# Kernel optimization log

Measured on AMD Instinct MI355X. Metric: run time of the kernel, lower is better.

The kernel has to match this reference:

```python
import jax, jax.numpy as jnp
import numpy as np

L = 2        # n_layer
D = 1024     # hidden_size
H = 8        # n_head
DK = D // H  # head_dim = 128
DV = D // H
T = 2048     # max_seq_length
B = 4
INTER = 2816 # fla GatedMLP: int(1024*4*2/3)=2730 rounded up to multiple of 256
EPS = 1e-6


def rmsnorm(x, w):
    return x * jax.lax.rsqrt(jnp.mean(x * x, axis=-1, keepdims=True) + EPS) * w


def l2norm(x):
    return x * jax.lax.rsqrt(jnp.sum(x * x, axis=-1, keepdims=True) + EPS)


def delta_attn(x, Wq, Wk, Wv, Wb, Wo, onorm_w):
    # x: [B, T, D]
    b, t, _ = x.shape
    q = jax.nn.silu((x @ Wq).reshape(b, t, H, DK))
    k = jax.nn.silu((x @ Wk).reshape(b, t, H, DK))
    q = l2norm(q)
    k = l2norm(k)
    v = jax.nn.silu((x @ Wv).reshape(b, t, H, DV))
    beta = jax.nn.sigmoid(x @ Wb) * 2.0  # [B,T,H], allow_neg_eigval=True
    # time-major for scan
    qt = q.transpose(1, 0, 2, 3)  # [T,B,H,DK]
    kt = k.transpose(1, 0, 2, 3)
    vt = v.transpose(1, 0, 2, 3)
    bt = beta.transpose(1, 0, 2)  # [T,B,H]

    def step(S, inps):
        qi, ki, vi, bi = inps
        # delta rule: S_t = S_{t-1} + beta_t * k_t (v_t - S_{t-1}^T k_t)^T
        pred = jnp.einsum('bhkv,bhk->bhv', S, ki)
        S = S + bi[..., None, None] * ki[..., :, None] * (vi - pred)[..., None, :]
        o = jnp.einsum('bhkv,bhk->bhv', S, qi)
        return S, o

    S0 = jnp.zeros((b, H, DK, DV), x.dtype)
    _, o = jax.lax.scan(step, S0, (qt, kt, vt, bt))  # o: [T,B,H,DV]
    o = rmsnorm(o, onorm_w)  # per-head RMSNorm (use_gate=False)
    o = o.transpose(1, 0, 2, 3).reshape(b, t, H * DV)
    return o @ Wo


def setup_inputs() -> dict:
    key = jax.random.key(0)
    ks = jax.random.split(key, 13)
    s = 0.02
    f32 = jnp.float32
    return {
        'input_embeds': jax.random.normal(ks[0], (T, B, D), f32),
        'Wq': jax.random.normal(ks[1], (L, D, D), f32) * s,
        'Wk': jax.random.normal(ks[2], (L, D, D), f32) * s,
        'Wv': jax.random.normal(ks[3], (L, D, D), f32) * s,
        'Wb': jax.random.normal(ks[4], (L, D, H), f32) * s,
        'Wo': jax.random.normal(ks[5], (L, D, D), f32) * s,
        'onorm_w': jnp.ones((L, DV), f32) + jax.random.normal(ks[6], (L, DV), f32) * 0.02,
        'norm1_w': jnp.ones((L, D), f32) + jax.random.normal(ks[7], (L, D), f32) * 0.02,
        'norm2_w': jnp.ones((L, D), f32) + jax.random.normal(ks[8], (L, D), f32) * 0.02,
        'Wg': jax.random.normal(ks[9], (L, D, 2 * INTER), f32) * s,
        'Wd': jax.random.normal(ks[10], (L, INTER, D), f32) * s,
        'final_norm_w': jnp.ones((D,), f32) + jax.random.normal(ks[11], (D,), f32) * 0.02,
    }


def reference(input_embeds, Wq, Wk, Wv, Wb, Wo, onorm_w, norm1_w, norm2_w, Wg, Wd, final_norm_w):
    # wrapper transposes (T,B,D) -> (B,T,D)
    x = input_embeds.transpose(1, 0, 2)
    for l in range(L):
        h = rmsnorm(x, norm1_w[l])
        x = x + delta_attn(h, Wq[l], Wk[l], Wv[l], Wb[l], Wo[l], onorm_w[l])
        h = rmsnorm(x, norm2_w[l])
        gy = h @ Wg[l]
        g, y = jnp.split(gy, 2, axis=-1)
        x = x + (jax.nn.silu(g) * y) @ Wd[l]
    x = rmsnorm(x, final_norm_w)
    return x.transpose(1, 0, 2)  # back to (T,B,D)
```

## Files before the change

kernel.cpp:

```cpp
#include <hip/hip_runtime.h>
#include <hip/hip_bf16.h>
#include <cstdint>


typedef _Float16 f16;
typedef __attribute__((ext_vector_type(8))) _Float16 h8;
typedef __attribute__((ext_vector_type(4))) _Float16 h4;
typedef __attribute__((ext_vector_type(4))) float f4;

#define DEV __device__ __forceinline__

static constexpr int Bb_ = 4;
static constexpr int Hh  = 8;
static constexpr int Dd  = 1024;
static constexpr int Tt  = 2048;
static constexpr int NC  = 32;

DEV float siluf(float x) { return x / (1.f + expf(-x)); }
DEV int swz16(int row, int c) { return (c & 8) | ((c & 7) ^ (row & 7)); }

#define AS1(p) ((const __attribute__((address_space(1))) void*)(uintptr_t)(p))
#define AS3(p) ((__attribute__((address_space(3))) void*)(uint32_t)(uintptr_t)(p))

DEV h8 rd_sw(const f16* T, int row, int chunk) {
  return *(const h8*)(T + (((row << 3) | (chunk ^ (row & 7))) * 8));
}

template<int EPI, int BN>
__global__ __launch_bounds__(512, 2) void gemm2(const f16* __restrict__ A, const f16* __restrict__ Bt,
                                                void* __restrict__ C, int M, int N, int K, int gx) {
  __shared__ __align__(16) f16 ldsA[2][16384];
  __shared__ __align__(16) f16 ldsB[2][BN * 64];
  const int tid = threadIdx.x, lane = tid & 63, w = tid >> 6;
  const int l15 = lane & 15, l4 = lane >> 4;
  const int wr = w >> 2, wc = w & 3;
  const int nwg = gridDim.x;
  int flat = blockIdx.x;
  if ((nwg & 7) == 0) flat = (flat & 7) * (nwg >> 3) + (flat >> 3);
  const int bx = flat % gx, by = flat / gx;

  const f16* Ab = A + (size_t)by * 256 * K;
  const f16* Bb = Bt + (size_t)bx * BN * K;
  const int NT = K >> 6;
  constexpr int NCF = BN / 64;
  f4 acc[8][NCF] = {};

  const int r0 = tid >> 3;
  const size_t soff0 = (size_t)r0 * K + (size_t)(((tid & 7) ^ (r0 & 7)) * 8);
  const size_t soff1 = soff0 + (size_t)64 * K;
  const int dof = tid * 8;
  auto STG = [&](const f16* base, f16* dst) {
    __builtin_amdgcn_global_load_lds(AS1(base + soff0), AS3(dst + dof), 16, 0, 0);
    __builtin_amdgcn_global_load_lds(AS1(base + soff1), AS3(dst + 4096 + dof), 16, 0, 0);
  };

  STG(Bb, ldsB[0]);
  if (BN == 256) STG(Bb + (size_t)128 * K, ldsB[0] + 8192);
  STG(Ab, ldsA[0]);
  STG(Ab + (size_t)128 * K, ldsA[0] + 8192);
  if (NT > 1) {
    STG(Bb + 64, ldsB[1]);
    if (BN == 256) STG(Bb + (size_t)128 * K + 64, ldsB[1] + 8192);
    if (BN == 256) asm volatile("s_waitcnt vmcnt(4)");
    else           asm volatile("s_waitcnt vmcnt(2)");
  } else {
    asm volatile("s_waitcnt vmcnt(0)");
  }
  __builtin_amdgcn_s_barrier();

  for (int t = 0; t < NT; ++t) {
    const int cur = t & 1, nxt = cur ^ 1;
    const f16* cA = ldsA[cur];
    const f16* cB = ldsB[cur];
    h8 b[NCF][2];
    h8 a[2][2];
#pragma unroll
    for (int cf = 0; cf < NCF; ++cf)
#pragma unroll
      for (int ks = 0; ks < 2; ++ks)
        b[cf][ks] = rd_sw(cB, wc * (BN / 4) + cf * 16 + l15, ks * 4 + l4);
#pragma unroll
    for (int fr = 0; fr < 2; ++fr)
#pragma unroll
      for (int ks = 0; ks < 2; ++ks)
        a[fr][ks] = rd_sw(cA, wr * 128 + fr * 16 + l15, ks * 4 + l4);
    if (t + 1 < NT) STG(Ab + (t + 1) * 64, ldsA[nxt]);
    asm volatile("s_waitcnt lgkmcnt(0)");
    __builtin_amdgcn_s_setprio(1);
#pragma unroll
    for (int fr = 0; fr < 2; ++fr)
#pragma unroll
      for (int cf = 0; cf < NCF; ++cf)
#pragma unroll
        for (int ks = 0; ks < 2; ++ks)
          acc[fr][cf] = __builtin_amdgcn_mfma_f32_16x16x32_f16(a[fr][ks], b[cf][ks], acc[fr][cf], 0, 0, 0);
    __builtin_amdgcn_s_setprio(0);
    __builtin_amdgcn_s_barrier();
#pragma unroll
    for (int p = 1; p < 4; ++p) {
#pragma unroll
      for (int fr = 0; fr < 2; ++fr)
#pragma unroll
        for (int ks = 0; ks < 2; ++ks)
          a[fr][ks] = rd_sw(cA, wr * 128 + p * 32 + fr * 16 + l15, ks * 4 + l4);
      if (p == 1 && t + 1 < NT) STG(Ab + (size_t)128 * K + (t + 1) * 64, ldsA[nxt] + 8192);
      if (p == 2 && t + 2 < NT) STG(Bb + (t + 2) * 64, ldsB[cur]);
      if (BN == 256 && p == 3 && t + 2 < NT) STG(Bb + (size_t)128 * K + (t + 2) * 64, ldsB[cur] + 8192);
      asm volatile("s_waitcnt lgkmcnt(0)");
      __builtin_amdgcn_s_setprio(1);
#pragma unroll
      for (int fr = 0; fr < 2; ++fr)
#pragma unroll
        for (int cf = 0; cf < NCF; ++cf)
#pragma unroll
          for (int ks = 0; ks < 2; ++ks)
            acc[p * 2 + fr][cf] = __builtin_amdgcn_mfma_f32_16x16x32_f16(a[fr][ks], b[cf][ks], acc[p * 2 + fr][cf], 0, 0, 0);
      __builtin_amdgcn_s_setprio(0);
      if (p == 3) {
        if (t + 2 < NT) {
          if (BN == 256) asm volatile("s_waitcnt vmcnt(4)");
          else           asm volatile("s_waitcnt vmcnt(2)");
        } else if (t + 1 < NT) {
          asm volatile("s_waitcnt vmcnt(0)");
        }
      }
      __builtin_amdgcn_s_barrier();
    }
  }

#pragma unroll
  for (int fr = 0; fr < 8; ++fr) {
#pragma unroll
    for (int cf = 0; cf < NCF; ++cf) {
      const int row0 = by * 256 + wr * 128 + fr * 16 + l4 * 4;
      const int col = bx * BN + wc * (BN / 4) + cf * 16 + l15;
#pragma unroll
      for (int q = 0; q < 4; ++q) {
        const size_t idx = (size_t)(row0 + q) * N + col;
        const float v = acc[fr][cf][q];
        if (EPI == 0) ((float*)C)[idx] = v;
        if (EPI == 1) ((f16*)C)[idx] = (f16)((float)((f16*)C)[idx] + v);
        if (EPI == 2) ((f16*)C)[idx] = (f16)v;
      }
    }
  }
}

__global__ __launch_bounds__(512, 2) void gemmGLU(const f16* __restrict__ A, const f16* __restrict__ WgT,
                                                  f16* __restrict__ my, int K, int gx) {
  __shared__ __align__(16) f16 ldsA[2][16384];
  __shared__ __align__(16) f16 ldsG[2][8192];
  __shared__ __align__(16) f16 ldsY[2][8192];
  const int tid = threadIdx.x, lane = tid & 63, w = tid >> 6;
  const int l15 = lane & 15, l4 = lane >> 4;
  const int wr = w >> 2, wc = w & 3;
  const int nwg = gridDim.x;
  int flat = blockIdx.x;
  if ((nwg & 7) == 0) flat = (flat & 7) * (nwg >> 3) + (flat >> 3);
  const int bx = flat % gx, by = flat / gx;

  const f16* Ab = A + (size_t)by * 256 * K;
  const f16* Gb = WgT + (size_t)bx * 128 * K;
  const f16* Yb = WgT + (size_t)(2816 + bx * 128) * K;
  const int NT = K >> 6;
  f4 accG[8][2] = {}, accY[8][2] = {};

  const int r0 = tid >> 3;
  const size_t soff0 = (size_t)r0 * K + (size_t)(((tid & 7) ^ (r0 & 7)) * 8);
  const size_t soff1 = soff0 + (size_t)64 * K;
  const int dof = tid * 8;
  auto STG = [&](const f16* base, f16* dst) {
    __builtin_amdgcn_global_load_lds(AS1(base + soff0), AS3(dst + dof), 16, 0, 0);
    __builtin_amdgcn_global_load_lds(AS1(base + soff1), AS3(dst + 4096 + dof), 16, 0, 0);
  };

  STG(Gb, ldsG[0]);
  STG(Yb, ldsY[0]);
  STG(Ab, ldsA[0]);
  STG(Ab + (size_t)128 * K, ldsA[0] + 8192);
  if (NT > 1) {
    STG(Gb + 64, ldsG[1]);
    STG(Yb + 64, ldsY[1]);
    asm volatile("s_waitcnt vmcnt(4)");
  } else {
    asm volatile("s_waitcnt vmcnt(0)");
  }
  __builtin_amdgcn_s_barrier();

  for (int t = 0; t < NT; ++t) {
    const int cur = t & 1, nxt = cur ^ 1;
    const f16* cA = ldsA[cur];
    h8 bg[2][2], byv[2][2];
    h8 a[2][2];
#pragma unroll
    for (int cf = 0; cf < 2; ++cf)
#pragma unroll
      for (int ks = 0; ks < 2; ++ks) {
        bg[cf][ks] = rd_sw(ldsG[cur], wc * 32 + cf * 16 + l15, ks * 4 + l4);
        byv[cf][ks] = rd_sw(ldsY[cur], wc * 32 + cf * 16 + l15, ks * 4 + l4);
      }
#pragma unroll
    for (int fr = 0; fr < 2; ++fr)
#pragma unroll
      for (int ks = 0; ks < 2; ++ks)
        a[fr][ks] = rd_sw(cA, wr * 128 + fr * 16 + l15, ks * 4 + l4);
    if (t + 1 < NT) STG(Ab + (t + 1) * 64, ldsA[nxt]);
    asm volatile("s_waitcnt lgkmcnt(0)");
    __builtin_amdgcn_s_setprio(1);
#pragma unroll
    for (int fr = 0; fr < 2; ++fr)
#pragma unroll
      for (int cf = 0; cf < 2; ++cf)
#pragma unroll
        for (int ks = 0; ks < 2; ++ks) {
          accG[fr][cf] = __builtin_amdgcn_mfma_f32_16x16x32_f16(a[fr][ks], bg[cf][ks], accG[fr][cf], 0, 0, 0);
          accY[fr][cf] = __builtin_amdgcn_mfma_f32_16x16x32_f16(a[fr][ks], byv[cf][ks], accY[fr][cf], 0, 0, 0);
        }
    __builtin_amdgcn_s_setprio(0);
    __builtin_amdgcn_s_barrier();
#pragma unroll
    for (int p = 1; p < 4; ++p) {
#pragma unroll
      for (int fr = 0; fr < 2; ++fr)
#pragma unroll
        for (int ks = 0; ks < 2; ++ks)
          a[fr][ks] = rd_sw(cA, wr * 128 + p * 32 + fr * 16 + l15, ks * 4 + l4);
      if (p == 1 && t + 1 < NT) STG(Ab + (size_t)128 * K + (t + 1) * 64, ldsA[nxt] + 8192);
      if (p == 2 && t + 2 < NT) STG(Gb + (t + 2) * 64, ldsG[cur]);
      if (p == 3 && t + 2 < NT) STG(Yb + (t + 2) * 64, ldsY[cur]);
      asm volatile("s_waitcnt lgkmcnt(0)");
      __builtin_amdgcn_s_setprio(1);
#pragma unroll
      for (int fr = 0; fr < 2; ++fr)
#pragma unroll
        for (int cf = 0; cf < 2; ++cf)
#pragma unroll
          for (int ks = 0; ks < 2; ++ks) {
            accG[p * 2 + fr][cf] = __builtin_amdgcn_mfma_f32_16x16x32_f16(a[fr][ks], bg[cf][ks], accG[p * 2 + fr][cf], 0, 0, 0);
            accY[p * 2 + fr][cf] = __builtin_amdgcn_mfma_f32_16x16x32_f16(a[fr][ks], byv[cf][ks], accY[p * 2 + fr][cf], 0, 0, 0);
          }
      __builtin_amdgcn_s_setprio(0);
      if (p == 3) {
        if (t + 2 < NT) asm volatile("s_waitcnt vmcnt(4)");
        else if (t + 1 < NT) asm volatile("s_waitcnt vmcnt(0)");
      }
      __builtin_amdgcn_s_barrier();
    }
  }

#pragma unroll
  for (int fr = 0; fr < 8; ++fr) {
#pragma unroll
    for (int cf = 0; cf < 2; ++cf) {
      const int row0 = by * 256 + wr * 128 + fr * 16 + l4 * 4;
      const int col = bx * 128 + wc * 32 + cf * 16 + l15;
#pragma unroll
      for (int q = 0; q < 4; ++q)
        my[(size_t)(row0 + q) * 2816 + col] = (f16)(siluf(accG[fr][cf][q]) * accY[fr][cf][q]);
    }
  }
}

__global__ __launch_bounds__(256) void cvt_k(const float* __restrict__ in, f16* __restrict__ out) {
  const size_t i = ((size_t)blockIdx.x * 256 + threadIdx.x) * 8;
  const float4 a = *(const float4*)(in + i);
  const float4 b = *(const float4*)(in + i + 4);
  h8 o = {(f16)a.x, (f16)a.y, (f16)a.z, (f16)a.w, (f16)b.x, (f16)b.y, (f16)b.z, (f16)b.w};
  *(h8*)(out + i) = o;
}

template<int OUT_F16>
__global__ __launch_bounds__(256) void rmsnorm_k(const f16* __restrict__ x, const float* __restrict__ w,
                                                 void* __restrict__ out) {
  const int r = blockIdx.x, tid = threadIdx.x;
  const h4 xv = *(const h4*)(x + (size_t)r * 1024 + tid * 4);
  const float v0 = (float)xv[0], v1 = (float)xv[1], v2 = (float)xv[2], v3 = (float)xv[3];
  float ss = v0 * v0 + v1 * v1 + v2 * v2 + v3 * v3;
#pragma unroll
  for (int m = 1; m < 64; m <<= 1) ss += __shfl_xor(ss, m);
  __shared__ float red[4];
  if ((tid & 63) == 0) red[tid >> 6] = ss;
  __syncthreads();
  const float scale = rsqrtf((red[0] + red[1] + red[2] + red[3]) * (1.f / 1024.f) + 1e-6f);
  const float4 w4 = *(const float4*)(w + tid * 4);
  float o0 = v0 * scale * w4.x, o1 = v1 * scale * w4.y, o2 = v2 * scale * w4.z, o3 = v3 * scale * w4.w;
  if (OUT_F16) {
    h4 o = {(f16)o0, (f16)o1, (f16)o2, (f16)o3};
    *(h4*)((f16*)out + (size_t)r * 1024 + tid * 4) = o;
  } else {
    *(float4*)((float*)out + (size_t)r * 1024 + tid * 4) = make_float4(o0, o1, o2, o3);
  }
}

__global__ __launch_bounds__(256) void qkv_epi(const f16* __restrict__ qkv, f16* __restrict__ qb,
                                               f16* __restrict__ kb, f16* __restrict__ vb) {
  const int r = blockIdx.x, tid = threadIdx.x;
  const int head = tid >> 5, l32 = tid & 31;
  const int i = (r >> 2) & 63;
  const size_t src = (size_t)r * 3072 + head * 128 + l32 * 4;
  {
    const h4 v = *(const h4*)(qkv + src);
    float s0 = siluf((float)v[0]), s1 = siluf((float)v[1]), s2 = siluf((float)v[2]), s3 = siluf((float)v[3]);
    float ss = s0 * s0 + s1 * s1 + s2 * s2 + s3 * s3;
#pragma unroll
    for (int m = 1; m <= 16; m <<= 1) ss += __shfl_xor(ss, m);
    const float sc = rsqrtf(ss + 1e-6f);
    h4 o = {(f16)(s0 * sc), (f16)(s1 * sc), (f16)(s2 * sc), (f16)(s3 * sc)};
    const int c = l32 >> 1, off = (l32 & 1) * 4;
    *(h4*)(qb + (size_t)r * 1024 + head * 128 + swz16(i, c) * 8 + off) = o;
  }
  {
    const h4 v = *(const h4*)(qkv + src + 1024);
    float s0 = siluf((float)v[0]), s1 = siluf((float)v[1]), s2 = siluf((float)v[2]), s3 = siluf((float)v[3]);
    float ss = s0 * s0 + s1 * s1 + s2 * s2 + s3 * s3;
#pragma unroll
    for (int m = 1; m <= 16; m <<= 1) ss += __shfl_xor(ss, m);
    const float sc = rsqrtf(ss + 1e-6f);
    h4 o = {(f16)(s0 * sc), (f16)(s1 * sc), (f16)(s2 * sc), (f16)(s3 * sc)};
    const int c = l32 >> 1, off = (l32 & 1) * 4;
    *(h4*)(kb + (size_t)r * 1024 + head * 128 + swz16(i, c) * 8 + off) = o;
  }
  {
    const h4 v = *(const h4*)(qkv + (size_t)r * 3072 + 2048 + tid * 4);
    h4 o = {(f16)siluf((float)v[0]), (f16)siluf((float)v[1]), (f16)siluf((float)v[2]), (f16)siluf((float)v[3])};
    const int hd = tid >> 5, dh = (tid & 31) * 4;
    const int c = dh >> 3, off = dh & 7;
    *(h4*)(vb + (size_t)r * 1024 + hd * 128 + swz16(i, c) * 8 + off) = o;
  }
}

__global__ __launch_bounds__(256) void onorm_k(const f16* __restrict__ o, const float* __restrict__ w,
                                               f16* __restrict__ ob) {
  const int r = blockIdx.x, tid = threadIdx.x;
  const int head = tid >> 5, l32 = tid & 31;
  const size_t base = (size_t)r * 1024 + head * 128 + l32 * 4;
  const h4 xv = *(const h4*)(o + base);
  const float v0 = (float)xv[0], v1 = (float)xv[1], v2 = (float)xv[2], v3 = (float)xv[3];
  float ss = v0 * v0 + v1 * v1 + v2 * v2 + v3 * v3;
#pragma unroll
  for (int m = 1; m <= 16; m <<= 1) ss += __shfl_xor(ss, m);
  const float sc = rsqrtf(ss * (1.f / 128.f) + 1e-6f);
  const float4 w4 = *(const float4*)(w + l32 * 4);
  h4 out = {(f16)(v0 * sc * w4.x), (f16)(v1 * sc * w4.y), (f16)(v2 * sc * w4.z), (f16)(v3 * sc * w4.w)};
  *(h4*)(ob + base) = out;
}

__global__ __launch_bounds__(256) void beta_k(const f16* __restrict__ hb, const float* __restrict__ Wb,
                                              float* __restrict__ beta) {
  const int tid = threadIdx.x, lane = tid & 63, wv = tid >> 6;
  const int r = blockIdx.x * 4 + wv;
  const f16* row = hb + (size_t)r * 1024 + lane * 16;
  const h8 v0 = *(const h8*)(row);
  const h8 v1 = *(const h8*)(row + 8);
  const float* wb = Wb + (size_t)(lane * 16) * 8;
  float acc[8] = {};
#pragma unroll
  for (int e = 0; e < 8; ++e) {
    const float x0 = (float)v0[e], x1 = (float)v1[e];
    const float4 w0a = *(const float4*)(wb + e * 8);
    const float4 w0b = *(const float4*)(wb + e * 8 + 4);
    const float4 w1a = *(const float4*)(wb + (e + 8) * 8);
    const float4 w1b = *(const float4*)(wb + (e + 8) * 8 + 4);
    acc[0] += x0 * w0a.x + x1 * w1a.x;  acc[1] += x0 * w0a.y + x1 * w1a.y;
    acc[2] += x0 * w0a.z + x1 * w1a.z;  acc[3] += x0 * w0a.w + x1 * w1a.w;
    acc[4] += x0 * w0b.x + x1 * w1b.x;  acc[5] += x0 * w0b.y + x1 * w1b.y;
    acc[6] += x0 * w0b.z + x1 * w1b.z;  acc[7] += x0 * w0b.w + x1 * w1b.w;
  }
#pragma unroll
  for (int j = 0; j < 8; ++j)
#pragma unroll
    for (int m = 1; m < 64; m <<= 1) acc[j] += __shfl_xor(acc[j], m);
  if (lane == 0) {
#pragma unroll
    for (int j = 0; j < 8; ++j) beta[(size_t)r * 8 + j] = 2.f / (1.f + expf(-acc[j]));
  }
}

__global__ __launch_bounds__(256) void transpose_k(const float* __restrict__ W, f16* __restrict__ Wt,
                                                   int K, int N) {
  __shared__ float tile[32][33];
  const int n0 = blockIdx.x * 32, k0 = blockIdx.y * 32;
  const int tx = threadIdx.x & 31, ty = threadIdx.x >> 5;
#pragma unroll
  for (int i = 0; i < 32; i += 8) tile[ty + i][tx] = W[(size_t)(k0 + ty + i) * N + n0 + tx];
  __syncthreads();
#pragma unroll
  for (int i = 0; i < 32; i += 8) Wt[(size_t)(n0 + ty + i) * K + k0 + tx] = (f16)tile[tx][ty + i];
}

__global__ void fill_k(float* p, int n, float v) {
  const int i = blockIdx.x * 256 + threadIdx.x;
  if (i < n) p[i] = v;
}

DEV f4 mm16(const f16* A, int as, const f16* B, f4 c, int l15, int l4) {
  h4 a = *(const h4*)(A + l15 * as + l4 * 4);
  h4 b = *(const h4*)(B + l15 * 20 + l4 * 4);
  return __builtin_amdgcn_mfma_f32_16x16x16f16(a, b, c, 0, 0, 0);
}
DEV void wr_T(f16* slot, f4 acc, int l15, int l4, float sgn) {
  h4 v = {(f16)(sgn * acc[0]), (f16)(sgn * acc[1]), (f16)(sgn * acc[2]), (f16)(sgn * acc[3])};
  *(h4*)(slot + l15 * 20 + l4 * 4) = v;
}
DEV void wr_Tb(f16* Tb, int bi, int bj, f4 acc, const float* betas, int l15, int l4, float sgn) {
  const float bc = betas[bj * 16 + l15];
#pragma unroll
  for (int q = 0; q < 4; ++q)
    Tb[(bi * 16 + l4 * 4 + q) * 72 + bj * 16 + l15] = (f16)(sgn * acc[q] * bc);
}

__global__ __launch_bounds__(256) void phaseA(const f16* __restrict__ kb, const f16* __restrict__ qb,
                                              const f16* __restrict__ vb, const float* __restrict__ beta,
                                              f16* __restrict__ wbuf, f16* __restrict__ utbuf,
                                              f16* __restrict__ pbuf, f16* __restrict__ ktbuf) {
  const int blk = blockIdx.x;
  const int c = blk >> 5, bh = blk & 31;
  const int b = bh >> 3, h = bh & 7;
  const int tid = threadIdx.x, lane = tid & 63, wv = tid >> 6;
  const int l15 = lane & 15, l4 = lane >> 4;

  __shared__ __align__(16) f16 Ks[64 * 128];
  __shared__ __align__(16) f16 QVs[64 * 128];
  __shared__ __align__(16) f16 Abuf[64 * 68];
  __shared__ __align__(16) f16 Dr[4][16 * 20];
  __shared__ __align__(16) f16 Dt[4][16 * 20];
  __shared__ __align__(16) f16 Tp[3][16 * 20];
  __shared__ __align__(16) f16 Xp[3][16 * 20];
  __shared__ __align__(16) f16 Tb[64 * 72];
  __shared__ float betas[64];

  const size_t rowstr = (size_t)Bb_ * Dd;
  const size_t gbase = ((size_t)(c * 64) * Bb_ + b) * Dd + h * 128;

#pragma unroll
  for (int i = 0; i < 4; ++i) {
    const int ch = tid + i * 256;
    const int rr = ch >> 4, kc = ch & 15;
    *(h8*)(Ks + ch * 8) = *(const h8*)(kb + gbase + (size_t)rr * rowstr + kc * 8);
    *(h8*)(QVs + ch * 8) = *(const h8*)(qb + gbase + (size_t)rr * rowstr + kc * 8);
  }
  for (int i = tid; i < 64 * 72; i += 256) Tb[i] = (f16)0.f;
  if (tid < 64) betas[tid] = beta[((size_t)(c * 64 + tid) * Bb_ + b) * Hh + h];
  __syncthreads();

  f4 accS[4] = {}, accP[4] = {};
  const int arow = wv * 16 + l15;
#pragma unroll
  for (int kc = 0; kc < 4; ++kc) {
    const int c4 = kc * 4 + l4;
    const h8 aK = *(const h8*)(Ks + arow * 128 + swz16(arow, c4) * 8);
    const h8 aQ = *(const h8*)(QVs + arow * 128 + swz16(arow, c4) * 8);
#pragma unroll
    for (int f = 0; f < 4; ++f) {
      const int brow = f * 16 + l15;
      const h8 bK = *(const h8*)(Ks + brow * 128 + swz16(brow, c4) * 8);
      accS[f] = __builtin_amdgcn_mfma_f32_16x16x32_f16(aK, bK, accS[f], 0, 0, 0);
      accP[f] = __builtin_amdgcn_mfma_f32_16x16x32_f16(aQ, bK, accP[f], 0, 0, 0);
    }
  }
  const size_t pbase = (((size_t)bh * NC + c) * 64) * 64;
#pragma unroll
  for (int f = 0; f < 4; ++f) {
#pragma unroll
    for (int q = 0; q < 4; ++q) {
      const int i = wv * 16 + l4 * 4 + q;
      const int j = f * 16 + l15;
      Abuf[i * 68 + j] = (f16)((j < i) ? betas[i] * accS[f][q] : 0.f);
      pbuf[pbase + (size_t)i * 64 + j] = (f16)((j <= i) ? accP[f][q] : 0.f);
    }
  }
// ... 181 lines not shown
    if (c + 1 < NC) asm volatile("s_waitcnt vmcnt(12)" ::: "memory");
    else            asm volatile("s_waitcnt vmcnt(0)" ::: "memory");
#pragma unroll
    for (int f = 0; f < 2; ++f) {
      const h4 uu = f ? u1 : u0;
      h4 rw;
#pragma unroll
      for (int q = 0; q < 4; ++q) {
        const float rv = (float)uu[q] - accR[f][q];
        accR[f][q] = rv;
        rw[q] = (f16)rv;
      }
      *(h4*)(Rt + (f * 16 + l15) * 72 + wv * 16 + l4 * 4) = rw;
    }
    asm volatile("s_waitcnt lgkmcnt(0)" ::: "memory");
    __builtin_amdgcn_s_barrier();

#pragma unroll
    for (int kc = 0; kc < 2; ++kc) {
      const h8 aP = kc ? aP1 : aP0;
#pragma unroll
      for (int f = 0; f < 2; ++f) {
        const h8 bR = *(const h8*)(Rt + (f * 16 + l15) * 72 + kc * 32 + koff);
        accO[f] = __builtin_amdgcn_mfma_f32_16x16x32_f16(aP, bR, accO[f], 0, 0, 0);
      }
    }
#pragma unroll
    for (int f = 0; f < 2; ++f)
#pragma unroll
      for (int q = 0; q < 4; ++q) {
        const int i = wv * 16 + l4 * 4 + q;
        const int cc = f * 16 + l15;
        obuf[((size_t)(c * 64 + i) * Bb_ + b) * Dd + h * 128 + g * 32 + cc] = (f16)accO[f][q];
      }

#pragma unroll
    for (int kc = 0; kc < 2; ++kc) {
      const h8 aR0 = *(const h8*)(Rt + l15 * 72 + kc * 32 + koff);
      const h8 aR1 = *(const h8*)(Rt + (16 + l15) * 72 + kc * 32 + koff);
#pragma unroll
      for (int cf = 0; cf < 2; ++cf) {
        const int kcol = wv * 32 + cf * 16 + l15;
        const int c2 = kc * 4 + l4;
        const h8 bKv = *(const h8*)(Kts[cur] + kcol * 64 + (c2 ^ (kcol & 7)) * 8);
        macc[0][cf] = __builtin_amdgcn_mfma_f32_16x16x32_f16(aR0, bKv, macc[0][cf], 0, 0, 0);
        macc[1][cf] = __builtin_amdgcn_mfma_f32_16x16x32_f16(aR1, bKv, macc[1][cf], 0, 0, 0);
      }
    }
#pragma unroll
    for (int rf = 0; rf < 2; ++rf)
#pragma unroll
      for (int cf = 0; cf < 2; ++cf)
#pragma unroll
        for (int q = 0; q < 4; ++q) {
          const int cr = rf * 16 + l4 * 4 + q;
          const int kcol = wv * 32 + cf * 16 + l15;
          Ms[cr * 136 + kcol] = (f16)macc[rf][cf][q];
        }
  }
}

extern "C" void kernel_launch(void* const* d_in, const int* in_sizes, int n_in,
                              void* d_out, int out_size, void* d_ws, size_t ws_size,
                              hipStream_t stream) {
  (void)in_sizes; (void)n_in;
  const float* input = (const float*)d_in[0];
  const float* Wq = (const float*)d_in[1];
  const float* Wk = (const float*)d_in[2];
  const float* Wv = (const float*)d_in[3];
  const float* Wb = (const float*)d_in[4];
  const float* Wo = (const float*)d_in[5];
  const float* onw = (const float*)d_in[6];
  const float* n1w = (const float*)d_in[7];
  const float* n2w = (const float*)d_in[8];
  const float* Wg = (const float*)d_in[9];
  const float* Wd = (const float*)d_in[10];
  const float* fnw = (const float*)d_in[11];

  char* ws = (char*)d_ws;
  size_t off = 0;
  auto alloc = [&](size_t bytes) { void* p = ws + off; off += (bytes + 255) & ~(size_t)255; return p; };
  const size_t RD = 8192ull * 1024ull;
  f16*  x     = (f16*)alloc(RD * 2);
  f16*  hb    = (f16*)alloc(RD * 2);
  f16*  qb    = (f16*)alloc(RD * 2);
  f16*  kbuf  = (f16*)alloc(RD * 2);
  f16*  vbuf  = (f16*)alloc(RD * 2);
  float* beta = (float*)alloc(8192ull * 8 * 4);
  f16*  wbuf  = (f16*)alloc(RD * 2);
  f16*  utbuf = (f16*)alloc(RD * 2);
  f16*  ktbuf = (f16*)alloc(RD * 2);
  f16*  pbuf  = (f16*)alloc(32ull * 32 * 64 * 64 * 2);
  char* arena = (char*)alloc(3 * RD * 2);
  f16*  WqkvT = (f16*)alloc(3072ull * 1024 * 2);
  f16*  WoT   = (f16*)alloc(1024ull * 1024 * 2);
  f16*  WgT   = (f16*)alloc(5632ull * 1024 * 2);
  f16*  WdT   = (f16*)alloc(1024ull * 2816 * 2);
  if (off > ws_size) {
    fill_k<<<(out_size + 255) / 256, 256, 0, stream>>>((float*)d_out, out_size, 1.0e6f);
    return;
  }
  f16* qkvraw = (f16*)arena;
  f16* obuf = (f16*)arena;
  f16* my = qb;
  f16* ob = wbuf;

  cvt_k<<<4096, 256, 0, stream>>>(input, x);

  for (int l = 0; l < 2; ++l) {
    const size_t o2 = (size_t)l * 1024 * 1024;
    transpose_k<<<dim3(32, 32), 256, 0, stream>>>(Wq + o2, WqkvT, 1024, 1024);
    transpose_k<<<dim3(32, 32), 256, 0, stream>>>(Wk + o2, WqkvT + 1024ull * 1024, 1024, 1024);
    transpose_k<<<dim3(32, 32), 256, 0, stream>>>(Wv + o2, WqkvT + 2048ull * 1024, 1024, 1024);
    transpose_k<<<dim3(32, 32), 256, 0, stream>>>(Wo + o2, WoT, 1024, 1024);
    transpose_k<<<dim3(176, 32), 256, 0, stream>>>(Wg + (size_t)l * 1024 * 5632, WgT, 1024, 5632);
    transpose_k<<<dim3(32, 88), 256, 0, stream>>>(Wd + (size_t)l * 2816 * 1024, WdT, 2816, 1024);

    rmsnorm_k<1><<<8192, 256, 0, stream>>>(x, n1w + l * 1024, hb);
    gemm2<2, 128><<<32 * 24, 512, 0, stream>>>(hb, WqkvT, qkvraw, 8192, 3072, 1024, 24);
    beta_k<<<2048, 256, 0, stream>>>(hb, Wb + (size_t)l * 1024 * 8, beta);
    qkv_epi<<<8192, 256, 0, stream>>>(qkvraw, qb, kbuf, vbuf);
    phaseA<<<1024, 256, 0, stream>>>(kbuf, qb, vbuf, beta, wbuf, utbuf, pbuf, ktbuf);
    phaseB<<<128, 256, 0, stream>>>(qb, ktbuf, wbuf, utbuf, pbuf, obuf);
    onorm_k<<<8192, 256, 0, stream>>>(obuf, onw + l * 128, ob);
    gemm2<1, 128><<<32 * 8, 512, 0, stream>>>(ob, WoT, x, 8192, 1024, 1024, 8);

    rmsnorm_k<1><<<8192, 256, 0, stream>>>(x, n2w + l * 1024, hb);
    gemmGLU<<<32 * 22, 512, 0, stream>>>(hb, WgT, my, 1024, 22);
    gemm2<1, 128><<<32 * 8, 512, 0, stream>>>(my, WdT, x, 8192, 1024, 2816, 8);
  }
  rmsnorm_k<0><<<8192, 256, 0, stream>>>(x, fnw, d_out);
}
```

Baseline: 993.7 us.

## Fold RMSNorm into GEMM weights and row-scale epilogue; restructure GEMM K-loop

Removes the materialized normalized activation buffer. The norm weights are folded into the transposed projection weights, and a small kernel computes per-row inverse RMS scales. The QKV, GLU and beta GEMMs then apply that scale in their epilogue. The GEMM main loops are also restructured from four barrier-separated phases into two halves, with double register buffers and fewer lgkmcnt waits and barriers. This saves a full read/write pass over the activations but relies on the compiler to order LDS reads, since the explicit lgkmcnt waits are gone.

```diff
diff --git a/kernel.cpp b/kernel.cpp
--- a/kernel.cpp
+++ b/kernel.cpp
@@ -26,11 +26,12 @@
   return *(const h8*)(T + (((row << 3) | (chunk ^ (row & 7))) * 8));
 }
 
-template<int EPI, int BN>
+template<int EPI, int SC>
 __global__ __launch_bounds__(512, 2) void gemm2(const f16* __restrict__ A, const f16* __restrict__ Bt,
-                                                void* __restrict__ C, int M, int N, int K, int gx) {
+                                                void* __restrict__ C, const float* __restrict__ rs,
+                                                int M, int N, int K, int gx) {
   __shared__ __align__(16) f16 ldsA[2][16384];
-  __shared__ __align__(16) f16 ldsB[2][BN * 64];
+  __shared__ __align__(16) f16 ldsB[2][8192];
   const int tid = threadIdx.x, lane = tid & 63, w = tid >> 6;
   const int l15 = lane & 15, l4 = lane >> 4;
   const int wr = w >> 2, wc = w & 3;
@@ -40,10 +41,9 @@
   const int bx = flat % gx, by = flat / gx;
 
   const f16* Ab = A + (size_t)by * 256 * K;
-  const f16* Bb = Bt + (size_t)bx * BN * K;
+  const f16* Bb = Bt + (size_t)bx * 128 * K;
   const int NT = K >> 6;
-  constexpr int NCF = BN / 64;
-  f4 acc[8][NCF] = {};
+  f4 acc[8][2] = {};
 
   const int r0 = tid >> 3;
   const size_t soff0 = (size_t)r0 * K + (size_t)(((tid & 7) ^ (r0 & 7)) * 8);
@@ -55,14 +55,11 @@
   };
 
   STG(Bb, ldsB[0]);
-  if (BN == 256) STG(Bb + (size_t)128 * K, ldsB[0] + 8192);
   STG(Ab, ldsA[0]);
   STG(Ab + (size_t)128 * K, ldsA[0] + 8192);
   if (NT > 1) {
     STG(Bb + 64, ldsB[1]);
-    if (BN == 256) STG(Bb + (size_t)128 * K + 64, ldsB[1] + 8192);
-    if (BN == 256) asm volatile("s_waitcnt vmcnt(4)");
-    else           asm volatile("s_waitcnt vmcnt(2)");
+    asm volatile("s_waitcnt vmcnt(2)");
   } else {
     asm volatile("s_waitcnt vmcnt(0)");
   }
@@ -72,73 +69,83 @@
     const int cur = t & 1, nxt = cur ^ 1;
     const f16* cA = ldsA[cur];
     const f16* cB = ldsB[cur];
-    h8 b[NCF][2];
-    h8 a[2][2];
-#pragma unroll
-    for (int cf = 0; cf < NCF; ++cf)
+    h8 b[2][2], aX[2][2], aY[2][2];
+#pragma unroll
+    for (int cf = 0; cf < 2; ++cf)
 #pragma unroll
       for (int ks = 0; ks < 2; ++ks)
-        b[cf][ks] = rd_sw(cB, wc * (BN / 4) + cf * 16 + l15, ks * 4 + l4);
+        b[cf][ks] = rd_sw(cB, wc * 32 + cf * 16 + l15, ks * 4 + l4);
 #pragma unroll
     for (int fr = 0; fr < 2; ++fr)
 #pragma unroll
       for (int ks = 0; ks < 2; ++ks)
-        a[fr][ks] = rd_sw(cA, wr * 128 + fr * 16 + l15, ks * 4 + l4);
-    if (t + 1 < NT) STG(Ab + (t + 1) * 64, ldsA[nxt]);
-    asm volatile("s_waitcnt lgkmcnt(0)");
+        aX[fr][ks] = rd_sw(cA, wr * 128 + fr * 16 + l15, ks * 4 + l4);
+    if (t + 1 < NT) { STG(Ab + (t + 1) * 64, ldsA[nxt]); STG(Ab + (size_t)128 * K + (t + 1) * 64, ldsA[nxt] + 8192); }
     __builtin_amdgcn_s_setprio(1);
 #pragma unroll
     for (int fr = 0; fr < 2; ++fr)
 #pragma unroll
-      for (int cf = 0; cf < NCF; ++cf)
+      for (int cf = 0; cf < 2; ++cf)
 #pragma unroll
         for (int ks = 0; ks < 2; ++ks)
-          acc[fr][cf] = __builtin_amdgcn_mfma_f32_16x16x32_f16(a[fr][ks], b[cf][ks], acc[fr][cf], 0, 0, 0);
+          acc[fr][cf] = __builtin_amdgcn_mfma_f32_16x16x32_f16(aX[fr][ks], b[cf][ks], acc[fr][cf], 0, 0, 0);
+#pragma unroll
+    for (int fr = 0; fr < 2; ++fr)
+#pragma unroll
+      for (int ks = 0; ks < 2; ++ks)
+        aY[fr][ks] = rd_sw(cA, wr * 128 + 32 + fr * 16 + l15, ks * 4 + l4);
+#pragma unroll
+    for (int fr = 0; fr < 2; ++fr)
+#pragma unroll
+      for (int cf = 0; cf < 2; ++cf)
+#pragma unroll
+        for (int ks = 0; ks < 2; ++ks)
+          acc[2 + fr][cf] = __builtin_amdgcn_mfma_f32_16x16x32_f16(aY[fr][ks], b[cf][ks], acc[2 + fr][cf], 0, 0, 0);
     __builtin_amdgcn_s_setprio(0);
     __builtin_amdgcn_s_barrier();
 #pragma unroll
-    for (int p = 1; p < 4; ++p) {
-#pragma unroll
-      for (int fr = 0; fr < 2; ++fr)
+    for (int fr = 0; fr < 2; ++fr)
+#pragma unroll
+      for (int ks = 0; ks < 2; ++ks)
+        aX[fr][ks] = rd_sw(cA, wr * 128 + 64 + fr * 16 + l15, ks * 4 + l4);
+    if (t + 2 < NT) STG(Bb + (t + 2) * 64, ldsB[cur]);
+    __builtin_amdgcn_s_setprio(1);
+#pragma unroll
+    for (int fr = 0; fr < 2; ++fr)
+#pragma unroll
+      for (int cf = 0; cf < 2; ++cf)
 #pragma unroll
         for (int ks = 0; ks < 2; ++ks)
-          a[fr][ks] = rd_sw(cA, wr * 128 + p * 32 + fr * 16 + l15, ks * 4 + l4);
-      if (p == 1 && t + 1 < NT) STG(Ab + (size_t)128 * K + (t + 1) * 64, ldsA[nxt] + 8192);
-      if (p == 2 && t + 2 < NT) STG(Bb + (t + 2) * 64, ldsB[cur]);
-      if (BN == 256 && p == 3 && t + 2 < NT) STG(Bb + (size_t)128 * K + (t + 2) * 64, ldsB[cur] + 8192);
-      asm volatile("s_waitcnt lgkmcnt(0)");
-      __builtin_amdgcn_s_setprio(1);
-#pragma unroll
-      for (int fr = 0; fr < 2; ++fr)
-#pragma unroll
-        for (int cf = 0; cf < NCF; ++cf)
-#pragma unroll
-          for (int ks = 0; ks < 2; ++ks)
-            acc[p * 2 + fr][cf] = __builtin_amdgcn_mfma_f32_16x16x32_f16(a[fr][ks], b[cf][ks], acc[p * 2 + fr][cf], 0, 0, 0);
-      __builtin_amdgcn_s_setprio(0);
-      if (p == 3) {
-        if (t + 2 < NT) {
-          if (BN == 256) asm volatile("s_waitcnt vmcnt(4)");
-          else           asm volatile("s_waitcnt vmcnt(2)");
-        } else if (t + 1 < NT) {
-          asm volatile("s_waitcnt vmcnt(0)");
-        }
-      }
-      __builtin_amdgcn_s_barrier();
-    }
+          acc[4 + fr][cf] = __builtin_amdgcn_mfma_f32_16x16x32_f16(aX[fr][ks], b[cf][ks], acc[4 + fr][cf], 0, 0, 0);
+#pragma unroll
+    for (int fr = 0; fr < 2; ++fr)
+#pragma unroll
+      for (int ks = 0; ks < 2; ++ks)
+        aY[fr][ks] = rd_sw(cA, wr * 128 + 96 + fr * 16 + l15, ks * 4 + l4);
+#pragma unroll
+    for (int fr = 0; fr < 2; ++fr)
+#pragma unroll
+      for (int cf = 0; cf < 2; ++cf)
+#pragma unroll
+        for (int ks = 0; ks < 2; ++ks)
+          acc[6 + fr][cf] = __builtin_amdgcn_mfma_f32_16x16x32_f16(aY[fr][ks], b[cf][ks], acc[6 + fr][cf], 0, 0, 0);
+    __builtin_amdgcn_s_setprio(0);
+    if (t + 2 < NT)      asm volatile("s_waitcnt vmcnt(2)" ::: "memory");
+    else if (t + 1 < NT) asm volatile("s_waitcnt vmcnt(0)" ::: "memory");
+    __builtin_amdgcn_s_barrier();
   }
 
 #pragma unroll
   for (int fr = 0; fr < 8; ++fr) {
 #pragma unroll
-    for (int cf = 0; cf < NCF; ++cf) {
+    for (int cf = 0; cf < 2; ++cf) {
       const int row0 = by * 256 + wr * 128 + fr * 16 + l4 * 4;
-      const int col = bx * BN + wc * (BN / 4) + cf * 16 + l15;
+      const int col = bx * 128 + wc * 32 + cf * 16 + l15;
 #pragma unroll
       for (int q = 0; q < 4; ++q) {
         const size_t idx = (size_t)(row0 + q) * N + col;
-        const float v = acc[fr][cf][q];
-        if (EPI == 0) ((float*)C)[idx] = v;
+        float v = acc[fr][cf][q];
+        if (SC) v *= rs[row0 + q];
         if (EPI == 1) ((f16*)C)[idx] = (f16)((float)((f16*)C)[idx] + v);
         if (EPI == 2) ((f16*)C)[idx] = (f16)v;
       }
@@ -147,7 +154,8 @@
 }
 
 __global__ __launch_bounds__(512, 2) void gemmGLU(const f16* __restrict__ A, const f16* __restrict__ WgT,
-                                                  f16* __restrict__ my, int K, int gx) {
+                                                  const float* __restrict__ rs, f16* __restrict__ my,
+                                                  int K, int gx) {
   __shared__ __align__(16) f16 ldsA[2][16384];
   __shared__ __align__(16) f16 ldsG[2][8192];
   __shared__ __align__(16) f16 ldsY[2][8192];
@@ -190,8 +198,7 @@
   for (int t = 0; t < NT; ++t) {
     const int cur = t & 1, nxt = cur ^ 1;
     const f16* cA = ldsA[cur];
-    h8 bg[2][2], byv[2][2];
-    h8 a[2][2];
+    h8 bg[2][2], byv[2][2], aX[2][2], aY[2][2];
 #pragma unroll
     for (int cf = 0; cf < 2; ++cf)
 #pragma unroll
@@ -203,9 +210,8 @@
     for (int fr = 0; fr < 2; ++fr)
 #pragma unroll
       for (int ks = 0; ks < 2; ++ks)
-        a[fr][ks] = rd_sw(cA, wr * 128 + fr * 16 + l15, ks * 4 + l4);
-    if (t + 1 < NT) STG(Ab + (t + 1) * 64, ldsA[nxt]);
-    asm volatile("s_waitcnt lgkmcnt(0)");
+        aX[fr][ks] = rd_sw(cA, wr * 128 + fr * 16 + l15, ks * 4 + l4);
+    if (t + 1 < NT) { STG(Ab + (t + 1) * 64, ldsA[nxt]); STG(Ab + (size_t)128 * K + (t + 1) * 64, ldsA[nxt] + 8192); }
     __builtin_amdgcn_s_setprio(1);
 #pragma unroll
     for (int fr = 0; fr < 2; ++fr)
@@ -213,39 +219,59 @@
       for (int cf = 0; cf < 2; ++cf)
 #pragma unroll
         for (int ks = 0; ks < 2; ++ks) {
-          accG[fr][cf] = __builtin_amdgcn_mfma_f32_16x16x32_f16(a[fr][ks], bg[cf][ks], accG[fr][cf], 0, 0, 0);
-          accY[fr][cf] = __builtin_amdgcn_mfma_f32_16x16x32_f16(a[fr][ks], byv[cf][ks], accY[fr][cf], 0, 0, 0);
+          accG[fr][cf] = __builtin_amdgcn_mfma_f32_16x16x32_f16(aX[fr][ks], bg[cf][ks], accG[fr][cf], 0, 0, 0);
+          accY[fr][cf] = __builtin_amdgcn_mfma_f32_16x16x32_f16(aX[fr][ks], byv[cf][ks], accY[fr][cf], 0, 0, 0);
+        }
+#pragma unroll
+    for (int fr = 0; fr < 2; ++fr)
+#pragma unroll
+      for (int ks = 0; ks < 2; ++ks)
+        aY[fr][ks] = rd_sw(cA, wr * 128 + 32 + fr * 16 + l15, ks * 4 + l4);
+#pragma unroll
+    for (int fr = 0; fr < 2; ++fr)
+#pragma unroll
+      for (int cf = 0; cf < 2; ++cf)
+#pragma unroll
+        for (int ks = 0; ks < 2; ++ks) {
+          accG[2 + fr][cf] = __builtin_amdgcn_mfma_f32_16x16x32_f16(aY[fr][ks], bg[cf][ks], accG[2 + fr][cf], 0, 0, 0);
+          accY[2 + fr][cf] = __builtin_amdgcn_mfma_f32_16x16x32_f16(aY[fr][ks], byv[cf][ks], accY[2 + fr][cf], 0, 0, 0);
         }
     __builtin_amdgcn_s_setprio(0);
     __builtin_amdgcn_s_barrier();
 #pragma unroll
-    for (int p = 1; p < 4; ++p) {
-#pragma unroll
-      for (int fr = 0; fr < 2; ++fr)
-#pragma unroll
-        for (int ks = 0; ks < 2; ++ks)
-          a[fr][ks] = rd_sw(cA, wr * 128 + p * 32 + fr * 16 + l15, ks * 4 + l4);
-      if (p == 1 && t + 1 < NT) STG(Ab + (size_t)128 * K + (t + 1) * 64, ldsA[nxt] + 8192);
-      if (p == 2 && t + 2 < NT) STG(Gb + (t + 2) * 64, ldsG[cur]);
-      if (p == 3 && t + 2 < NT) STG(Yb + (t + 2) * 64, ldsY[cur]);
-      asm volatile("s_waitcnt lgkmcnt(0)");
-      __builtin_amdgcn_s_setprio(1);
-#pragma unroll
-      for (int fr = 0; fr < 2; ++fr)
-#pragma unroll
-        for (int cf = 0; cf < 2; ++cf)
-#pragma unroll
-          for (int ks = 0; ks < 2; ++ks) {
-            accG[p * 2 + fr][cf] = __builtin_amdgcn_mfma_f32_16x16x32_f16(a[fr][ks], bg[cf][ks], accG[p * 2 + fr][cf], 0, 0, 0);
-            accY[p * 2 + fr][cf] = __builtin_amdgcn_mfma_f32_16x16x32_f16(a[fr][ks], byv[cf][ks], accY[p * 2 + fr][cf], 0, 0, 0);
-          }
-      __builtin_amdgcn_s_setprio(0);
-      if (p == 3) {
-        if (t + 2 < NT) asm volatile("s_waitcnt vmcnt(4)");
-        else if (t + 1 < NT) asm volatile("s_waitcnt vmcnt(0)");
-      }
-      __builtin_amdgcn_s_barrier();
-    }
+    for (int fr = 0; fr < 2; ++fr)
+#pragma unroll
+      for (int ks = 0; ks < 2; ++ks)
+        aX[fr][ks] = rd_sw(cA, wr * 128 + 64 + fr * 16 + l15, ks * 4 + l4);
+    if (t + 2 < NT) { STG(Gb + (t + 2) * 64, ldsG[cur]); STG(Yb + (t + 2) * 64, ldsY[cur]); }
+    __builtin_amdgcn_s_setprio(1);
+#pragma unroll
+    for (int fr = 0; fr < 2; ++fr)
+#pragma unroll
+      for (int cf = 0; cf < 2; ++cf)
+#pragma unroll
+        for (int ks = 0; ks < 2; ++ks) {
+          accG[4 + fr][cf] = __builtin_amdgcn_mfma_f32_16x16x32_f16(aX[fr][ks], bg[cf][ks], accG[4 + fr][cf], 0, 0, 0);
+          accY[4 + fr][cf] = __builtin_amdgcn_mfma_f32_16x16x32_f16(aX[fr][ks], byv[cf][ks], accY[4 + fr][cf], 0, 0, 0);
+        }
+#pragma unroll
+    for (int fr = 0; fr < 2; ++fr)
+#pragma unroll
+      for (int ks = 0; ks < 2; ++ks)
+        aY[fr][ks] = rd_sw(cA, wr * 128 + 96 + fr * 16 + l15, ks * 4 + l4);
+#pragma unroll
+    for (int fr = 0; fr < 2; ++fr)
+#pragma unroll
+      for (int cf = 0; cf < 2; ++cf)
+#pragma unroll
+        for (int ks = 0; ks < 2; ++ks) {
+          accG[6 + fr][cf] = __builtin_amdgcn_mfma_f32_16x16x32_f16(aY[fr][ks], bg[cf][ks], accG[6 + fr][cf], 0, 0, 0);
+          accY[6 + fr][cf] = __builtin_amdgcn_mfma_f32_16x16x32_f16(aY[fr][ks], byv[cf][ks], accY[6 + fr][cf], 0, 0, 0);
+        }
+    __builtin_amdgcn_s_setprio(0);
+    if (t + 2 < NT)      asm volatile("s_waitcnt vmcnt(4)" ::: "memory");
+    else if (t + 1 < NT) asm volatile("s_waitcnt vmcnt(0)" ::: "memory");
+    __builtin_amdgcn_s_barrier();
   }
 
 #pragma unroll
@@ -255,8 +281,10 @@
       const int row0 = by * 256 + wr * 128 + fr * 16 + l4 * 4;
       const int col = bx * 128 + wc * 32 + cf * 16 + l15;
 #pragma unroll
-      for (int q = 0; q < 4; ++q)
-        my[(size_t)(row0 + q) * 2816 + col] = (f16)(siluf(accG[fr][cf][q]) * accY[fr][cf][q]);
+      for (int q = 0; q < 4; ++q) {
+        const float s = rs[row0 + q];
+        my[(size_t)(row0 + q) * 2816 + col] = (f16)(siluf(s * accG[fr][cf][q]) * (s * accY[fr][cf][q]));
+      }
     }
   }
 }
@@ -269,9 +297,25 @@
   *(h8*)(out + i) = o;
 }
 
-template<int OUT_F16>
-__global__ __launch_bounds__(256) void rmsnorm_k(const f16* __restrict__ x, const float* __restrict__ w,
-                                                 void* __restrict__ out) {
+__global__ __launch_bounds__(256) void rowscale_k(const f16* __restrict__ x, float* __restrict__ rs) {
+  const int tid = threadIdx.x, lane = tid & 63, wv = tid >> 6;
+  const int r = blockIdx.x * 4 + wv;
+  const f16* row = x + (size_t)r * 1024 + lane * 16;
+  const h8 v0 = *(const h8*)(row);
+  const h8 v1 = *(const h8*)(row + 8);
+  float ss = 0.f;
+#pragma unroll
+  for (int e = 0; e < 8; ++e) {
+    const float a = (float)v0[e], b = (float)v1[e];
+    ss += a * a + b * b;
+  }
+#pragma unroll
+  for (int m = 1; m < 64; m <<= 1) ss += __shfl_xor(ss, m);
+  if (lane == 0) rs[r] = rsqrtf(ss * (1.f / 1024.f) + 1e-6f);
+}
+
+__global__ __launch_bounds__(256) void rmsnorm_f(const f16* __restrict__ x, const float* __restrict__ w,
+                                                 float* __restrict__ out) {
   const int r = blockIdx.x, tid = threadIdx.x;
   const h4 xv = *(const h4*)(x + (size_t)r * 1024 + tid * 4);
   const float v0 = (float)xv[0], v1 = (float)xv[1], v2 = (float)xv[2], v3 = (float)xv[3];
@@ -283,13 +327,8 @@
   __syncthreads();
   const float scale = rsqrtf((red[0] + red[1] + red[2] + red[3]) * (1.f / 1024.f) + 1e-6f);
   const float4 w4 = *(const float4*)(w + tid * 4);
-  float o0 = v0 * scale * w4.x, o1 = v1 * scale * w4.y, o2 = v2 * scale * w4.z, o3 = v3 * scale * w4.w;
-  if (OUT_F16) {
-    h4 o = {(f16)o0, (f16)o1, (f16)o2, (f16)o3};
-    *(h4*)((f16*)out + (size_t)r * 1024 + tid * 4) = o;
-  } else {
-    *(float4*)((float*)out + (size_t)r * 1024 + tid * 4) = make_float4(o0, o1, o2, o3);
-  }
+  *(float4*)(out + (size_t)r * 1024 + tid * 4) =
+      make_float4(v0 * scale * w4.x, v1 * scale * w4.y, v2 * scale * w4.z, v3 * scale * w4.w);
 }
 
 __global__ __launch_bounds__(256) void qkv_epi(const f16* __restrict__ qkv, f16* __restrict__ qb,
@@ -345,14 +384,14 @@
   *(h4*)(ob + base) = out;
 }
 
-__global__ __launch_bounds__(256) void beta_k(const f16* __restrict__ hb, const float* __restrict__ Wb,
-                                              float* __restrict__ beta) {
+__global__ __launch_bounds__(256) void beta_k(const f16* __restrict__ x, const float* __restrict__ Wb2,
+                                              const float* __restrict__ rs, float* __restrict__ beta) {
   const int tid = threadIdx.x, lane = tid & 63, wv = tid >> 6;
   const int r = blockIdx.x * 4 + wv;
-  const f16* row = hb + (size_t)r * 1024 + lane * 16;
+  const f16* row = x + (size_t)r * 1024 + lane * 16;
   const h8 v0 = *(const h8*)(row);
   const h8 v1 = *(const h8*)(row + 8);
-  const float* wb = Wb + (size_t)(lane * 16) * 8;
+  const float* wb = Wb2 + (size_t)(lane * 16) * 8;
   float acc[8] = {};
 #pragma unroll
   for (int e = 0; e < 8; ++e) {
@@ -371,21 +410,33 @@
 #pragma unroll
     for (int m = 1; m < 64; m <<= 1) acc[j] += __shfl_xor(acc[j], m);
   if (lane == 0) {
-#pragma unroll
-    for (int j = 0; j < 8; ++j) beta[(size_t)r * 8 + j] = 2.f / (1.f + expf(-acc[j]));
-  }
-}
-
-__global__ __launch_bounds__(256) void transpose_k(const float* __restrict__ W, f16* __restrict__ Wt,
-                                                   int K, int N) {
+    const float s = rs[r];
+#pragma unroll
+    for (int j = 0; j < 8; ++j) beta[(size_t)r * 8 + j] = 2.f / (1.f + expf(-acc[j] * s));
+  }
+}
+
+template<int FOLD>
+__global__ __launch_bounds__(256) void transpose_k(const float* __restrict__ W, const float* __restrict__ rw,
+                                                   f16* __restrict__ Wt, int K, int N) {
   __shared__ float tile[32][33];
   const int n0 = blockIdx.x * 32, k0 = blockIdx.y * 32;
   const int tx = threadIdx.x & 31, ty = threadIdx.x >> 5;
 #pragma unroll
-  for (int i = 0; i < 32; i += 8) tile[ty + i][tx] = W[(size_t)(k0 + ty + i) * N + n0 + tx];
+  for (int i = 0; i < 32; i += 8) {
+    float v = W[(size_t)(k0 + ty + i) * N + n0 + tx];
+    if (FOLD) v *= rw[k0 + ty + i];
+    tile[ty + i][tx] = v;
+  }
   __syncthreads();
 #pragma unroll
   for (int i = 0; i < 32; i += 8) Wt[(size_t)(n0 + ty + i) * K + k0 + tx] = (f16)tile[tx][ty + i];
+}
+
+__global__ __launch_bounds__(256) void bweight_k(const float* __restrict__ Wb, const float* __restrict__ n1w,
+                                                 float* __restrict__ Wb2) {
+  const int idx = blockIdx.x * 256 + threadIdx.x;
+  Wb2[idx] = Wb[idx] * n1w[idx >> 3];
 }
 
 __global__ void fill_k(float* p, int n, float v) {
@@ -733,11 +784,12 @@
   auto alloc = [&](size_t bytes) { void* p = ws + off; off += (bytes + 255) & ~(size_t)255; return p; };
   const size_t RD = 8192ull * 1024ull;
   f16*  x     = (f16*)alloc(RD * 2);
-  f16*  hb    = (f16*)alloc(RD * 2);
   f16*  qb    = (f16*)alloc(RD * 2);
   f16*  kbuf  = (f16*)alloc(RD * 2);
   f16*  vbuf  = (f16*)alloc(RD * 2);
   float* beta = (float*)alloc(8192ull * 8 * 4);
+  float* rs   = (float*)alloc(8192ull * 4);
+  float* Wb2  = (float*)alloc(1024ull * 8 * 4);
   f16*  wbuf  = (f16*)alloc(RD * 2);
   f16*  utbuf = (f16*)alloc(RD * 2);
   f16*  ktbuf = (f16*)alloc(RD * 2);
@@ -760,25 +812,26 @@
 
   for (int l = 0; l < 2; ++l) {
     const size_t o2 = (size_t)l * 1024 * 1024;
-    transpose_k<<<dim3(32, 32), 256, 0, stream>>>(Wq + o2, WqkvT, 1024, 1024);
-    transpose_k<<<dim3(32, 32), 256, 0, stream>>>(Wk + o2, WqkvT + 1024ull * 1024, 1024, 1024);
-    transpose_k<<<dim3(32, 32), 256, 0, stream>>>(Wv + o2, WqkvT + 2048ull * 1024, 1024, 1024);
-    transpose_k<<<dim3(32, 32), 256, 0, stream>>>(Wo + o2, WoT, 1024, 1024);
-    transpose_k<<<dim3(176, 32), 256, 0, stream>>>(Wg + (size_t)l * 1024 * 5632, WgT, 1024, 5632);
-    transpose_k<<<dim3(32, 88), 256, 0, stream>>>(Wd + (size_t)l * 2816 * 1024, WdT, 2816, 1024);
-
-    rmsnorm_k<1><<<8192, 256, 0, stream>>>(x, n1w + l * 1024, hb);
-    gemm2<2, 128><<<32 * 24, 512, 0, stream>>>(hb, WqkvT, qkvraw, 8192, 3072, 1024, 24);
-    beta_k<<<2048, 256, 0, stream>>>(hb, Wb + (size_t)l * 1024 * 8, beta);
+    transpose_k<1><<<dim3(32, 32), 256, 0, stream>>>(Wq + o2, n1w + l * 1024, WqkvT, 1024, 1024);
+    transpose_k<1><<<dim3(32, 32), 256, 0, stream>>>(Wk + o2, n1w + l * 1024, WqkvT + 1024ull * 1024, 1024, 1024);
+    transpose_k<1><<<dim3(32, 32), 256, 0, stream>>>(Wv + o2, n1w + l * 1024, WqkvT + 2048ull * 1024, 1024, 1024);
+    transpose_k<0><<<dim3(32, 32), 256, 0, stream>>>(Wo + o2, nullptr, WoT, 1024, 1024);
+    transpose_k<1><<<dim3(176, 32), 256, 0, stream>>>(Wg + (size_t)l * 1024 * 5632, n2w + l * 1024, WgT, 1024, 5632);
+    transpose_k<0><<<dim3(32, 88), 256, 0, stream>>>(Wd + (size_t)l * 2816 * 1024, nullptr, WdT, 2816, 1024);
+    bweight_k<<<32, 256, 0, stream>>>(Wb + (size_t)l * 1024 * 8, n1w + l * 1024, Wb2);
+
+    rowscale_k<<<2048, 256, 0, stream>>>(x, rs);
+    gemm2<2, 1><<<32 * 24, 512, 0, stream>>>(x, WqkvT, qkvraw, rs, 8192, 3072, 1024, 24);
+    beta_k<<<2048, 256, 0, stream>>>(x, Wb2, rs, beta);
     qkv_epi<<<8192, 256, 0, stream>>>(qkvraw, qb, kbuf, vbuf);
     phaseA<<<1024, 256, 0, stream>>>(kbuf, qb, vbuf, beta, wbuf, utbuf, pbuf, ktbuf);
     phaseB<<<128, 256, 0, stream>>>(qb, ktbuf, wbuf, utbuf, pbuf, obuf);
     onorm_k<<<8192, 256, 0, stream>>>(obuf, onw + l * 128, ob);
-    gemm2<1, 128><<<32 * 8, 512, 0, stream>>>(ob, WoT, x, 8192, 1024, 1024, 8);
-
-    rmsnorm_k<1><<<8192, 256, 0, stream>>>(x, n2w + l * 1024, hb);
-    gemmGLU<<<32 * 22, 512, 0, stream>>>(hb, WgT, my, 1024, 22);
-    gemm2<1, 128><<<32 * 8, 512, 0, stream>>>(my, WdT, x, 8192, 1024, 2816, 8);
-  }
-  rmsnorm_k<0><<<8192, 256, 0, stream>>>(x, fnw, d_out);
-}
+    gemm2<1, 0><<<32 * 8, 512, 0, stream>>>(ob, WoT, x, nullptr, 8192, 1024, 1024, 8);
+
+    rowscale_k<<<2048, 256, 0, stream>>>(x, rs);
+    gemmGLU<<<32 * 22, 512, 0, stream>>>(x, WgT, rs, my, 1024, 22);
+    gemm2<1, 0><<<32 * 8, 512, 0, stream>>>(my, WdT, x, nullptr, 8192, 1024, 2816, 8);
+  }
+  rmsnorm_f<<<8192, 256, 0, stream>>>(x, fnw, (float*)d_out);
+}
```

New measurement: 989.2 us. Within noise of the previous version (-0.5%).
